# Kernel optimization log

Measured on AMD Instinct MI355X. Metric: run time of the kernel, lower is better.

Reference implementation:

```python
import jax, jax.numpy as jnp
import numpy as np

TAU = 20.0
TH = 1.0
K = 10.0


def _lif_scan(I):
    # I: [B, L] float. Sequential leaky-integrate-fire over time with
    # straight-through (surrogate sigmoid) spikes and detached hard reset.
    def step(v, It):
        v = v + (-v / TAU + It)
        s_soft = jax.nn.sigmoid(K * (v - TH))
        s_hard = (v >= TH).astype(v.dtype)
        # s_hard.detach() - s_soft.detach() + s_soft  (straight-through)
        s = s_soft + jax.lax.stop_gradient(s_hard - s_soft)
        v = v * (1.0 - jax.lax.stop_gradient(s_hard))
        return v, s

    B, L = I.shape
    v0 = jnp.zeros((B,), dtype=I.dtype)
    _, spikes_t = jax.lax.scan(step, v0, I.T)  # spikes_t: [L, B]
    return spikes_t.T  # [B, L]


def _soft_lat(spikes):
    L = spikes.shape[1]
    time = jnp.arange(L, dtype=spikes.dtype)
    w = spikes / (spikes.sum(axis=1, keepdims=True) + 1e-6)
    return (w * time).sum(axis=1)


def setup_inputs() -> dict:
    key = jax.random.key(0)
    I = jax.random.normal(key, (65536, 400), dtype=jnp.float32)
    return {"I": I}


def reference(I):
    spikes = _lif_scan(I)  # [B, L]
    hard_latency = jnp.argmax(spikes, axis=1)  # [B] int
    soft_latency = _soft_lat(spikes)  # [B] float
    return (spikes, hard_latency, soft_latency)
```

## Files before the change

### kernel.cpp

```cpp
#include <hip/hip_runtime.h>


#define L_LEN 400
#define TC 80
#define NC 5
#define F4C 20
#define BIG 0x7fffffff

__device__ __forceinline__ float div20(float v) {
    const float c = 0.05f;
    float q = v * c;
    float r = fmaf(-20.0f, q, v);
    return fmaf(r, c, q);
}

__device__ __forceinline__ void load_chunk(const float* __restrict__ I, int row,
                                           int c, float4* regs) {
#pragma unroll
    for (int k = 0; k < F4C; ++k)
        regs[k] = *reinterpret_cast<const float4*>(
            I + (size_t)row * L_LEN + c * TC + k * 4);
}

struct ScanState {
    float v;
    int num;
    int cnt;
    int first;
};

__device__ __forceinline__ void scan_chunk(const float4* in, int cbase,
                                           ScanState& st, unsigned* bw) {
    unsigned b0 = 0, b1 = 0, b2 = 0;
    int numL = 0;
#pragma unroll
    for (int k = 0; k < F4C; ++k) {
        float x[4] = {in[k].x, in[k].y, in[k].z, in[k].w};
#pragma unroll
        for (int m = 0; m < 4; ++m) {
            const int tl = k * 4 + m;
            float d  = x[m] - div20(st.v);
            float vn = st.v + d;
            bool fire = vn >= 1.0f;
            numL = fire ? numL + tl : numL;
            if (tl < 32)      b0 |= fire ? (1u << tl) : 0u;
            else if (tl < 64) b1 |= fire ? (1u << (tl - 32)) : 0u;
            else              b2 |= fire ? (1u << (tl - 64)) : 0u;
            st.v = fire ? 0.0f : vn;
        }
    }
    int cntC = __builtin_popcount(b0) + __builtin_popcount(b1) +
               __builtin_popcount(b2);
    int fl = b0 ? __builtin_ctz(b0)
           : (b1 ? 32 + __builtin_ctz(b1)
           : (b2 ? 64 + __builtin_ctz(b2) : -1));
    st.num += numL + cbase * cntC;
    st.cnt += cntC;
    st.first = min(st.first, fl >= 0 ? cbase + fl : BIG);
    bw[0] = b0; bw[1] = b1; bw[2] = b2;
}

__global__ __launch_bounds__(64, 1) void lif_kernel(const float* __restrict__ I,
                                                    float* __restrict__ spikes,
                                                    float* __restrict__ hard_lat,
                                                    float* __restrict__ soft_lat) {
    __shared__ unsigned bits[64][3];
    const int j = threadIdx.x;
    const int R0 = blockIdx.x * 64;
    const int row = R0 + j;

    float4 A[F4C], B[F4C];
    load_chunk(I, row, 0, A);
    load_chunk(I, row, 1, B);

    ScanState st;
    st.v = 0.0f; st.num = 0; st.cnt = 0; st.first = BIG;

    for (int c = 0; c < NC; ++c) {
        unsigned bw[3];
        if ((c & 1) == 0) {
            scan_chunk(A, c * TC, st, bw);
            if (c + 2 < NC) load_chunk(I, row, c + 2, A);
        } else {
            scan_chunk(B, c * TC, st, bw);
            if (c + 2 < NC) load_chunk(I, row, c + 2, B);
        }
        bits[j][0] = bw[0]; bits[j][1] = bw[1]; bits[j][2] = bw[2];
#pragma unroll
        for (int i = 0; i < F4C; ++i) {
            int flat = i * 64 + j;
            int rl = flat / F4C;
            int k  = flat % F4C;
            unsigned w = bits[rl][k >> 3];
            int sh = (4 * k) & 31;
            float4 s;
            s.x = (float)((w >> (sh + 0)) & 1u);
            s.y = (float)((w >> (sh + 1)) & 1u);
            s.z = (float)((w >> (sh + 2)) & 1u);
            s.w = (float)((w >> (sh + 3)) & 1u);
            *reinterpret_cast<float4*>(
                spikes + (size_t)(R0 + rl) * L_LEN + c * TC + k * 4) = s;
        }
    }

    hard_lat[row] = (float)(st.first == BIG ? 0 : st.first);
    soft_lat[row] = (float)st.num / ((float)st.cnt + 1e-6f);
}

extern "C" void kernel_launch(void* const* d_in, const int* in_sizes, int n_in,
                              void* d_out, int out_size, void* d_ws, size_t ws_size,
                              hipStream_t stream) {
    const float* I = (const float*)d_in[0];
    int B = in_sizes[0] / L_LEN;

    float* spk = (float*)d_out;
    float* hard = spk + (size_t)B * L_LEN;
    float* soft = hard + B;

    dim3 block(64);
    dim3 grid(B / 64);
    hipLaunchKernelGGL(lif_kernel, grid, block, 0, stream, I, spk, hard, soft);
}
```

Before: 42.24 us.

## Split scan and spike-store work across producer/consumer wavefronts

Each block now has two wavefronts: wave 0 loads inputs and runs the sequential LIF scan, and wave 1 expands the spike bitmasks and writes the float spike tensor. A double-buffered shared bitmask and __syncthreads let the stores of one chunk overlap the scan of the next. Stores also become nontemporal. The cost is a barrier per chunk, twice the threads per block, and wave 1 idling during the scan.

```diff
diff --git a/kernel.cpp b/kernel.cpp
--- a/kernel.cpp
+++ b/kernel.cpp
@@ -7,6 +7,8 @@
 #define F4C 20
 #define BIG 0x7fffffff
 
+typedef float f4 __attribute__((ext_vector_type(4)));
+
 __device__ __forceinline__ float div20(float v) {
     const float c = 0.05f;
     float q = v * c;
@@ -15,10 +17,10 @@
 }
 
 __device__ __forceinline__ void load_chunk(const float* __restrict__ I, int row,
-                                           int c, float4* regs) {
+                                           int c, f4* regs) {
 #pragma unroll
     for (int k = 0; k < F4C; ++k)
-        regs[k] = *reinterpret_cast<const float4*>(
+        regs[k] = *reinterpret_cast<const f4*>(
             I + (size_t)row * L_LEN + c * TC + k * 4);
 }
 
@@ -29,17 +31,17 @@
     int first;
 };
 
-__device__ __forceinline__ void scan_chunk(const float4* in, int cbase,
+__device__ __forceinline__ void scan_chunk(const f4* in, int cbase,
                                            ScanState& st, unsigned* bw) {
     unsigned b0 = 0, b1 = 0, b2 = 0;
     int numL = 0;
 #pragma unroll
     for (int k = 0; k < F4C; ++k) {
-        float x[4] = {in[k].x, in[k].y, in[k].z, in[k].w};
 #pragma unroll
         for (int m = 0; m < 4; ++m) {
             const int tl = k * 4 + m;
-            float d  = x[m] - div20(st.v);
+            float x = in[k][m];
+            float d  = x - div20(st.v);
             float vn = st.v + d;
             bool fire = vn >= 1.0f;
             numL = fire ? numL + tl : numL;
@@ -60,51 +62,63 @@
     bw[0] = b0; bw[1] = b1; bw[2] = b2;
 }
 
-__global__ __launch_bounds__(64, 1) void lif_kernel(const float* __restrict__ I,
-                                                    float* __restrict__ spikes,
-                                                    float* __restrict__ hard_lat,
-                                                    float* __restrict__ soft_lat) {
-    __shared__ unsigned bits[64][3];
-    const int j = threadIdx.x;
+__global__ __launch_bounds__(128, 2) void lif_kernel(const float* __restrict__ I,
+                                                     float* __restrict__ spikes,
+                                                     float* __restrict__ hard_lat,
+                                                     float* __restrict__ soft_lat) {
+    __shared__ unsigned bits[2][64][3];
+    const int lane = threadIdx.x & 63;
+    const int wid  = threadIdx.x >> 6;
     const int R0 = blockIdx.x * 64;
-    const int row = R0 + j;
+    const int row = R0 + lane;
 
-    float4 A[F4C], B[F4C];
-    load_chunk(I, row, 0, A);
-    load_chunk(I, row, 1, B);
-
+    f4 A[F4C], Bb[F4C];
     ScanState st;
     st.v = 0.0f; st.num = 0; st.cnt = 0; st.first = BIG;
 
+    if (wid == 0) {
+        load_chunk(I, row, 0, A);
+        load_chunk(I, row, 1, Bb);
+    }
+
     for (int c = 0; c < NC; ++c) {
-        unsigned bw[3];
-        if ((c & 1) == 0) {
-            scan_chunk(A, c * TC, st, bw);
-            if (c + 2 < NC) load_chunk(I, row, c + 2, A);
-        } else {
-            scan_chunk(B, c * TC, st, bw);
-            if (c + 2 < NC) load_chunk(I, row, c + 2, B);
+        if (wid == 0) {
+            unsigned bw[3];
+            if ((c & 1) == 0) {
+                scan_chunk(A, c * TC, st, bw);
+                if (c + 2 < NC) load_chunk(I, row, c + 2, A);
+            } else {
+                scan_chunk(Bb, c * TC, st, bw);
+                if (c + 2 < NC) load_chunk(I, row, c + 2, Bb);
+            }
+            bits[c & 1][lane][0] = bw[0];
+            bits[c & 1][lane][1] = bw[1];
+            bits[c & 1][lane][2] = bw[2];
         }
-        bits[j][0] = bw[0]; bits[j][1] = bw[1]; bits[j][2] = bw[2];
+        __syncthreads();
+        if (wid == 1) {
 #pragma unroll
-        for (int i = 0; i < F4C; ++i) {
-            int flat = i * 64 + j;
-            int rl = flat / F4C;
-            int k  = flat % F4C;
-            unsigned w = bits[rl][k >> 3];
-            int sh = (4 * k) & 31;
-            float4 s;
-            s.x = (float)((w >> (sh + 0)) & 1u);
-            s.y = (float)((w >> (sh + 1)) & 1u);
-            s.z = (float)((w >> (sh + 2)) & 1u);
-            s.w = (float)((w >> (sh + 3)) & 1u);
-            *reinterpret_cast<float4*>(
-                spikes + (size_t)(R0 + rl) * L_LEN + c * TC + k * 4) = s;
+            for (int i = 0; i < F4C; ++i) {
+                int flat = i * 64 + lane;
+                int rl = flat / F4C;
+                int k  = flat % F4C;
+                unsigned w = bits[c & 1][rl][k >> 3];
+                int sh = (4 * k) & 31;
+                f4 s;
+                s.x = (float)((w >> (sh + 0)) & 1u);
+                s.y = (float)((w >> (sh + 1)) & 1u);
+                s.z = (float)((w >> (sh + 2)) & 1u);
+                s.w = (float)((w >> (sh + 3)) & 1u);
+                __builtin_nontemporal_store(s, reinterpret_cast<f4*>(
+                    spikes + (size_t)(R0 + rl) * L_LEN + c * TC + k * 4));
+            }
         }
     }
 
-    hard_lat[row] = (float)(st.first == BIG ? 0 : st.first);
-    soft_lat[row] = (float)st.num / ((float)st.cnt + 1e-6f);
+    if (wid == 0) {
+        hard_lat[row] = (float)(st.first == BIG ? 0 : st.first);
+        soft_lat[row] = (float)st.num / ((float)st.cnt + 1e-6f);
+    }
 }
 
 extern "C" void kernel_launch(void* const* d_in, const int* in_sizes, int n_in,
@@ -117,7 +131,7 @@
     float* hard = spk + (size_t)B * L_LEN;
     float* soft = hard + B;
 
-    dim3 block(64);
+    dim3 block(128);
     dim3 grid(B / 64);
     hipLaunchKernelGGL(lif_kernel, grid, block, 0, stream, I, spk, hard, soft);
 }
```

Result: slower. 109.5 us (+159.1%).

## Coalesce input loads through XOR-swizzled LDS transpose instead of per-row loads

Applied to the files above, without the earlier changes.

Input chunks are now loaded with a coalesced pattern, where consecutive threads read consecutive 16-byte pieces across rows. They are staged through an XOR-swizzled shared-memory tile so each thread can still scan its own row. Previously each thread did strided per-row float4 loads. The double register buffer (two chunks in flight) becomes a single prefetched chunk plus LDS, which cuts register pressure but lowers prefetch depth. It also adds LDS traffic and a missing explicit barrier, since one wavefront per block relies on wave-synchronous behaviour.

```diff
diff --git a/kernel.cpp b/kernel.cpp
--- a/kernel.cpp
+++ b/kernel.cpp
@@ -5,7 +5,10 @@
 #define TC 80
 #define NC 5
 #define F4C 20
+#define PITCHF 96
 #define BIG 0x7fffffff
+
+typedef float f4 __attribute__((ext_vector_type(4)));
 
 __device__ __forceinline__ float div20(float v) {
     const float c = 0.05f;
@@ -14,97 +17,115 @@
     return fmaf(r, c, q);
 }
 
-__device__ __forceinline__ void load_chunk(const float* __restrict__ I, int row,
-                                           int c, float4* regs) {
-#pragma unroll
-    for (int k = 0; k < F4C; ++k)
-        regs[k] = *reinterpret_cast<const float4*>(
-            I + (size_t)row * L_LEN + c * TC + k * 4);
-}
-
-struct ScanState {
-    float v;
-    int num;
-    int cnt;
-    int first;
-};
-
-__device__ __forceinline__ void scan_chunk(const float4* in, int cbase,
-                                           ScanState& st, unsigned* bw) {
-    unsigned b0 = 0, b1 = 0, b2 = 0;
-    int numL = 0;
-#pragma unroll
-    for (int k = 0; k < F4C; ++k) {
-        float x[4] = {in[k].x, in[k].y, in[k].z, in[k].w};
-#pragma unroll
-        for (int m = 0; m < 4; ++m) {
-            const int tl = k * 4 + m;
-            float d  = x[m] - div20(st.v);
-            float vn = st.v + d;
-            bool fire = vn >= 1.0f;
-            numL = fire ? numL + tl : numL;
-            if (tl < 32)      b0 |= fire ? (1u << tl) : 0u;
-            else if (tl < 64) b1 |= fire ? (1u << (tl - 32)) : 0u;
-            else              b2 |= fire ? (1u << (tl - 64)) : 0u;
-            st.v = fire ? 0.0f : vn;
-        }
-    }
-    int cntC = __builtin_popcount(b0) + __builtin_popcount(b1) +
-               __builtin_popcount(b2);
-    int fl = b0 ? __builtin_ctz(b0)
-           : (b1 ? 32 + __builtin_ctz(b1)
-           : (b2 ? 64 + __builtin_ctz(b2) : -1));
-    st.num += numL + cbase * cntC;
-    st.cnt += cntC;
-    st.first = min(st.first, fl >= 0 ? cbase + fl : BIG);
-    bw[0] = b0; bw[1] = b1; bw[2] = b2;
-}
-
 __global__ __launch_bounds__(64, 1) void lif_kernel(const float* __restrict__ I,
                                                     float* __restrict__ spikes,
                                                     float* __restrict__ hard_lat,
                                                     float* __restrict__ soft_lat) {
-    __shared__ unsigned bits[64][3];
+    __shared__ float lds_in[64 * PITCHF];
+    __shared__ unsigned bitsb[64 * 3];
     const int j = threadIdx.x;
     const int R0 = blockIdx.x * 64;
-    const int row = R0 + j;
+    const char* Ib = (const char*)I + (size_t)R0 * 1600;
+    char* Sb = (char*)spikes + (size_t)R0 * 1600;
 
-    float4 A[F4C], B[F4C];
-    load_chunk(I, row, 0, A);
-    load_chunk(I, row, 1, B);
+    const int r0 = j / 20;
+    const int k0 = j - r0 * 20;
 
-    ScanState st;
-    st.v = 0.0f; st.num = 0; st.cnt = 0; st.first = BIG;
+    f4 regs[F4C];
+
+    auto load_coal = [&](int c, f4* rg) {
+        int r = r0, k = k0;
+        int off = r * 1600 + k * 16 + c * 320;
+#pragma unroll
+        for (int i = 0; i < F4C; ++i) {
+            rg[i] = *reinterpret_cast<const f4*>(Ib + off);
+            int kn = k + 4; bool cr = kn >= 20;
+            k = cr ? kn - 20 : kn;
+            r += cr ? 4 : 3;
+            off += cr ? 6144 : 4864;
+        }
+    };
+
+    auto write_lds = [&](const f4* rg) {
+        int r = r0, k = k0;
+#pragma unroll
+        for (int i = 0; i < F4C; ++i) {
+            *reinterpret_cast<f4*>(&lds_in[r * PITCHF + ((k ^ (r & 7)) << 2)]) = rg[i];
+            int kn = k + 4; bool cr = kn >= 20;
+            k = cr ? kn - 20 : kn;
+            r += cr ? 4 : 3;
+        }
+    };
+
+    load_coal(0, regs);
+    write_lds(regs);
+
+    float v = 0.0f;
+    int num = 0, cnt = 0, first = BIG;
+    float* myrow = &lds_in[j * PITCHF];
+    const int jx = j & 7;
 
     for (int c = 0; c < NC; ++c) {
-        unsigned bw[3];
-        if ((c & 1) == 0) {
-            scan_chunk(A, c * TC, st, bw);
-            if (c + 2 < NC) load_chunk(I, row, c + 2, A);
-        } else {
-            scan_chunk(B, c * TC, st, bw);
-            if (c + 2 < NC) load_chunk(I, row, c + 2, B);
+        if (c + 1 < NC) load_coal(c + 1, regs);
+
+        unsigned b0 = 0, b1 = 0, b2 = 0;
+        int numL = 0;
+#pragma unroll
+        for (int k = 0; k < F4C; ++k) {
+            f4 x4 = *reinterpret_cast<const f4*>(&myrow[((k ^ jx) << 2)]);
+#pragma unroll
+            for (int m = 0; m < 4; ++m) {
+                const int tl = k * 4 + m;
+                float x = x4[m];
+                float d  = x - div20(v);
+                float vn = v + d;
+                bool fire = vn >= 1.0f;
+                numL = fire ? numL + tl : numL;
+                if (tl < 32)      b0 |= fire ? (1u << tl) : 0u;
+                else if (tl < 64) b1 |= fire ? (1u << (tl - 32)) : 0u;
+                else              b2 |= fire ? (1u << (tl - 64)) : 0u;
+                v = fire ? 0.0f : vn;
+            }
         }
-        bits[j][0] = bw[0]; bits[j][1] = bw[1]; bits[j][2] = bw[2];
+        int cntC = __builtin_popcount(b0) + __builtin_popcount(b1) +
+                   __builtin_popcount(b2);
+        int fl = b0 ? __builtin_ctz(b0)
+               : (b1 ? 32 + __builtin_ctz(b1)
+               : (b2 ? 64 + __builtin_ctz(b2) : -1));
+        int cbase = c * TC;
+        num += numL + cbase * cntC;
+        cnt += cntC;
+        first = min(first, fl >= 0 ? cbase + fl : BIG);
+
+        bitsb[j * 3 + 0] = b0;
+        bitsb[j * 3 + 1] = b1;
+        bitsb[j * 3 + 2] = b2;
+        {
+            int r = r0, k = k0;
+            int off = r * 1600 + k * 16 + c * 320;
 #pragma unroll
-        for (int i = 0; i < F4C; ++i) {
-            int flat = i * 64 + j;
-            int rl = flat / F4C;
-            int k  = flat % F4C;
-            unsigned w = bits[rl][k >> 3];
-            int sh = (4 * k) & 31;
-            float4 s;
-            s.x = (float)((w >> (sh + 0)) & 1u);
-            s.y = (float)((w >> (sh + 1)) & 1u);
-            s.z = (float)((w >> (sh + 2)) & 1u);
-            s.w = (float)((w >> (sh + 3)) & 1u);
-            *reinterpret_cast<float4*>(
-                spikes + (size_t)(R0 + rl) * L_LEN + c * TC + k * 4) = s;
+            for (int i = 0; i < F4C; ++i) {
+                unsigned w = bitsb[r * 3 + (k >> 3)];
+                int sh = (k & 7) * 4;
+                f4 s;
+                s.x = (float)((w >> (sh + 0)) & 1u);
+                s.y = (float)((w >> (sh + 1)) & 1u);
+                s.z = (float)((w >> (sh + 2)) & 1u);
+                s.w = (float)((w >> (sh + 3)) & 1u);
+                *reinterpret_cast<f4*>(Sb + off) = s;
+                int kn = k + 4; bool cr = kn >= 20;
+                k = cr ? kn - 20 : kn;
+                r += cr ? 4 : 3;
+                off += cr ? 6144 : 4864;
+            }
         }
+
+        if (c + 1 < NC) write_lds(regs);
     }
 
-    hard_lat[row] = (float)(st.first == BIG ? 0 : st.first);
-    soft_lat[row] = (float)st.num / ((float)st.cnt + 1e-6f);
+    const int row = R0 + j;
+    hard_lat[row] = (float)(first == BIG ? 0 : first);
+    soft_lat[row] = (float)num / ((float)cnt + 1e-6f);
 }
 
 extern "C" void kernel_launch(void* const* d_in, const int* in_sizes, int n_in,
```

Measured after the change: 41.33 us. -2.1%, faster.
